# Kernel optimization log

Measured on AMD Instinct MI355X. Metric: run time of the kernel, lower is better.

Reference implementation:

```python
import jax, jax.numpy as jnp
import numpy as np

WIN = 9  # window_size (isotropic, module default)
EPS = 1e-5


def _box_sum3d(x, win):
    """Sum over a win^3 box, same-size output ('same' padding). x: [B,1,D,H,W].
    The ones kernel is separable, so apply three 1D convolutions."""
    pad = win // 2
    for ax in range(3):  # spatial axes D,H,W
        kshape = [1, 1, 1, 1, 1]
        kshape[2 + ax] = win
        k = jnp.ones(kshape, x.dtype)
        padding = [(0, 0)] * 3
        padding[ax] = (pad, pad)
        x = jax.lax.conv_general_dilated(x, k, window_strides=(1, 1, 1), padding=padding)
    return x


def setup_inputs() -> dict:
    key = jax.random.key(0)
    k1, k2 = jax.random.split(key)
    shape = (2, 1, 160, 192, 160)
    y_pred = jax.random.normal(k1, shape, dtype=jnp.float32)
    y_true = jax.random.normal(k2, shape, dtype=jnp.float32)
    return {"y_pred": y_pred, "y_true": y_true}


def reference(y_pred, y_true):
    I, J = y_true, y_pred
    win_size = jnp.asarray(WIN ** 3, I.dtype)  # 729

    I_sum = _box_sum3d(I, WIN)
    J_sum = _box_sum3d(J, WIN)
    I2_sum = _box_sum3d(I * I, WIN)
    J2_sum = _box_sum3d(J * J, WIN)
    IJ_sum = _box_sum3d(I * J, WIN)

    I_mean = I_sum / win_size
    J_mean = J_sum / win_size

    cross = IJ_sum - J_mean * I_sum - I_mean * J_sum + I_mean * J_mean * win_size
    I_var = I2_sum - 2 * I_mean * I_sum + I_mean * I_mean * win_size
    J_var = J2_sum - 2 * J_mean * J_sum + J_mean * J_mean * win_size

    cc = cross * cross / (I_var * J_var + EPS)
    return -jnp.mean(cc)
```

## Files before the change

### kernel.cpp

```cpp
#include <hip/hip_runtime.h>
#include <hip/hip_fp16.h>


#define B_    2
#define D_    160
#define H_    192
#define W_    160
#define HW_   (H_*W_)

#define RS    12
#define SLS   (24*RS)
#define FS    (2*SLS)
#define RAWSZ (5*FS)
#define ZROW  (2*RAWSZ)
#define ZEND  (ZROW + 16)
#define HSUM0 ZEND
#define HCS   160
#define HRS   10
#define HSZ   (10*HCS)
#define REDU  (HSUM0 + 2*HSZ)
#define SMEM  (REDU + 8)
#define DC    80
#define ZCH   (D_/DC)
#define NMAC  ((DC+8)/2)
#define W3I   (1.0f/729.0f)
#define NTOT  9830400.0f

#if __has_builtin(__builtin_amdgcn_rcpf)
#define RCP(x) __builtin_amdgcn_rcpf(x)
#else
#define RCP(x) (1.0f/(x))
#endif

typedef _Float16 half8 __attribute__((ext_vector_type(8)));
typedef float    f32x4 __attribute__((ext_vector_type(4)));
typedef unsigned u32x2 __attribute__((ext_vector_type(2)));
#define MFMA16(a,b,c) __builtin_amdgcn_mfma_f32_16x16x32_f16((a),(b),(c),0,0,0)

#if __has_builtin(__builtin_amdgcn_permlane32_swap)
#define PL32(a,b) do { u32x2 _s = __builtin_amdgcn_permlane32_swap((a),(b),false,false); \
                       (a)=_s[0]; (b)=_s[1]; } while(0)
#else
#define PL32(a,b) asm volatile("s_nop 1\nv_permlane32_swap_b32 %0, %1" : "+v"(a), "+v"(b))
#endif
#if __has_builtin(__builtin_amdgcn_permlane16_swap)
#define PL16(a,b) do { u32x2 _s = __builtin_amdgcn_permlane16_swap((a),(b),false,false); \
                       (a)=_s[0]; (b)=_s[1]; } while(0)
#else
#define PL16(a,b) asm volatile("s_nop 1\nv_permlane16_swap_b32 %0, %1" : "+v"(a), "+v"(b))
#endif

struct __align__(8) HP { __half2 a, b; };

__global__ __launch_bounds__(256, 4) void ncc_fused(const float* __restrict__ gI,
                                                    const float* __restrict__ gJ,
                                                    float* __restrict__ out)
{
  __shared__ __align__(16) float sm[SMEM];
  const int tid  = threadIdx.x;
  const int lane = tid & 63;
  const int Q    = tid >> 6;
  const int n15  = lane & 15;
  const int q4   = lane >> 4;
  const int w0   = blockIdx.x * 16;
  const int h0   = blockIdx.y * 16;
  const int bz   = blockIdx.z;
  const int bb   = bz / ZCH;
  const int d_lo = (bz % ZCH) * DC;

  for (int i = tid; i < ZEND; i += 256) sm[i] = 0.f;

  half8 SEL;
  #pragma unroll
  for (int j = 0; j < 8; ++j) {
    const int k = 8*q4 + j;
    SEL[j] = (k >= n15 && k <= n15 + 8) ? (_Float16)1 : (_Float16)0;
  }

  bool val0 = false, val1 = false;
  int  lo0 = 0, lo1 = 0, sc0 = 0, sc1 = 0;
  const float *pi0 = gI, *pj0 = gJ, *pi1 = gI, *pj1 = gJ;
  {
    auto prep = [&](int t, bool& val, int& lo, int& sc,
                    const float*& pi, const float*& pj) {
      if (t >= 288) { val = false; return; }
      sc = t / 144;
      const int u = t - sc*144;
      const int r = u / 6, c = u - r*6;
      const int gh = h0 - 4 + r, gw = w0 - 4 + 4*c;
      val = ((unsigned)gh < (unsigned)H_) && (gw >= 0) && (gw + 3 < W_);
      lo  = sc*SLS + r*RS + 2*c;
      const long off = ((long)(bb*D_ + (d_lo - 4 + sc))*H_ + gh)*(long)W_ + gw;
      pi = gI + off; pj = gJ + off;
    };
    prep(tid, val0, lo0, sc0, pi0, pj0);
    prep((tid >= 224) ? tid + 32 : 512, val1, lo1, sc1, pi1, pj1);
  }

  int rb_[3], hb_[3];
  #pragma unroll
  for (int i = 0; i < 3; ++i) {
    int c = Q + 4*i; if (c > 9) c = 9;
    rb_[i] = (c % 5)*FS + (c / 5)*SLS;
    hb_[i] = HSUM0 + c*HCS;
  }
  const int a1r = n15*RS + 4*q4;
  const int a2r = (n15 < 8) ? ((16 + n15)*RS + 4*q4) : -1;
  const int zr  = ZROW + 4*q4;

  const int rh = tid >> 4, rw = tid & 15;
  const int rbase = HSUM0 + rw*HRS + (rh >> 1);
  const int rsh   = (rh & 1) * 16;

  float ring[5][9], S[5];
  #pragma unroll
  for (int f = 0; f < 5; ++f) {
    S[f] = 0.f;
    #pragma unroll
    for (int k = 0; k < 9; ++k) ring[f][k] = 0.f;
  }
  float acc = 0.f;

  float4 f0i = {0,0,0,0}, f0j = {0,0,0,0}, f1i = {0,0,0,0}, f1j = {0,0,0,0};
  auto fetch = [&](int sbase) {
    if (val0 && (unsigned)(sbase + sc0) < (unsigned)D_) {
      f0i = *(const float4*)pi0; f0j = *(const float4*)pj0;
    } else { f0i = make_float4(0,0,0,0); f0j = make_float4(0,0,0,0); }
    pi0 += 2*HW_; pj0 += 2*HW_;
    if (val1 && (unsigned)(sbase + sc1) < (unsigned)D_) {
      f1i = *(const float4*)pi1; f1j = *(const float4*)pj1;
    } else { f1i = make_float4(0,0,0,0); f1j = make_float4(0,0,0,0); }
    pi1 += 2*HW_; pj1 += 2*HW_;
  };

  auto stage_one = [&](int lo, float4 fi, float4 fj) {
    const __half2 i01 = __floats2half2_rn(fi.x, fi.y);
    const __half2 i23 = __floats2half2_rn(fi.z, fi.w);
    const __half2 j01 = __floats2half2_rn(fj.x, fj.y);
    const __half2 j23 = __floats2half2_rn(fj.z, fj.w);
    HP hI; hI.a = i01; hI.b = i23;
    HP hJ; hJ.a = j01; hJ.b = j23;
    HP h2; h2.a = __hmul2(i01, i01); h2.b = __hmul2(i23, i23);
    HP h3; h3.a = __hmul2(j01, j01); h3.b = __hmul2(j23, j23);
    HP h4; h4.a = __hmul2(i01, j01); h4.b = __hmul2(i23, j23);
    *(HP*)&sm[lo]        = hI;
    *(HP*)&sm[lo +   FS] = hJ;
    *(HP*)&sm[lo + 2*FS] = h2;
    *(HP*)&sm[lo + 3*FS] = h3;
    *(HP*)&sm[lo + 4*FS] = h4;
  };
  auto stage_write = [&](int buf) {
    const int b = buf * RAWSZ;
    if (val0) stage_one(b + lo0, f0i, f0j);
    if (val1) stage_one(b + lo1, f1i, f1j);
  };

  auto chain = [&](int rb, int hb) {
    const half8 A1 = *(const half8*)&sm[rb + a1r];
    const half8 A2 = (a2r >= 0) ? *(const half8*)&sm[rb + a2r]
                                : *(const half8*)&sm[zr];
    const f32x4 z = {0.f, 0.f, 0.f, 0.f};
    const f32x4 d1 = MFMA16(A1, SEL, z);
    const f32x4 d2 = MFMA16(A2, SEL, z);
    unsigned t0 = __builtin_bit_cast(unsigned, __floats2half2_rn(d1[0], d1[1]));
    unsigned t1 = __builtin_bit_cast(unsigned, __floats2half2_rn(d1[2], d1[3]));
    unsigned u0 = __builtin_bit_cast(unsigned, __floats2half2_rn(d2[0], d2[1]));
    unsigned u1 = __builtin_bit_cast(unsigned, __floats2half2_rn(d2[2], d2[3]));
    PL32(t0, u0);
    PL32(t1, u1);
    PL16(t0, u0);
    PL16(t1, u1);
    union { unsigned u[4]; half8 h; } Bv;
    Bv.u[0] = t0; Bv.u[1] = t1; Bv.u[2] = u0; Bv.u[3] = u1;
    const f32x4 dh = MFMA16(SEL, Bv.h, z);
    HP ph; ph.a = __floats2half2_rn(dh[0], dh[1]); ph.b = __floats2half2_rn(dh[2], dh[3]);
    *(HP*)&sm[hb + n15*HRS + 2*q4] = ph;
  };

  auto h2ext = [&](int addr) -> float {
    const unsigned u = *(const unsigned*)&sm[addr];
    return __half2float(__ushort_as_half((unsigned short)(u >> rsh)));
  };
  auto ring_cc = [&](int m, int hB) {
    float nA[5], nB[5];
    #pragma unroll
    for (int f = 0; f < 5; ++f) {
      nA[f] = h2ext(rbase + hB + f*HCS);
      nB[f] = h2ext(rbase + hB + (5 + f)*HCS);
    }
    float SA[5], SB[5];
    #pragma unroll
    for (int f = 0; f < 5; ++f) {
      SA[f] = S[f]  + nA[f] - ring[f][8];
      SB[f] = SA[f] + nB[f] - ring[f][7];
      S[f]  = SB[f];
      #pragma unroll
      for (int k = 8; k >= 2; --k) ring[f][k] = ring[f][k-2];
      ring[f][1] = nA[f]; ring[f][0] = nB[f];
    }
    if (m >= 4) {
      {
        const float cr = SA[4] - SA[0]*SA[1]*W3I;
        const float vi = SA[2] - SA[0]*SA[0]*W3I;
        const float vj = SA[3] - SA[1]*SA[1]*W3I;
        acc += cr*cr * RCP(vi*vj + 1e-5f);
      }
      {
        const float cr = SB[4] - SB[0]*SB[1]*W3I;
        const float vi = SB[2] - SB[0]*SB[0]*W3I;
        const float vj = SB[3] - SB[1]*SB[1]*W3I;
        acc += cr*cr * RCP(vi*vj + 1e-5f);
      }
    }
  };

  fetch(d_lo - 4);
  __syncthreads();
  stage_write(0);
  fetch(d_lo - 2);
  __syncthreads();

  for (int m = 0; m < NMAC; ++m) {
    const int rB = (m & 1) * RAWSZ;
    const int hB = (m & 1) * HSZ;
    if (m + 1 < NMAC) { stage_write((m + 1) & 1); fetch(d_lo + 2*m); }
    chain(rB + rb_[0], hB + hb_[0]);
    chain(rB + rb_[1], hB + hb_[1]);
    if (Q < 2) chain(rB + rb_[2], hB + hb_[2]);
    __syncthreads();
    ring_cc(m, hB);
  }

  float v = acc;
  #pragma unroll
  for (int off = 32; off > 0; off >>= 1)
    v += __shfl_down(v, off, 64);
  if (lane == 0) sm[REDU + Q] = v;
  __syncthreads();
  if (tid == 0) {
    const float t = sm[REDU] + sm[REDU+1] + sm[REDU+2] + sm[REDU+3];
    atomicAdd(out, -t / NTOT);
  }
}

extern "C" void kernel_launch(void* const* d_in, const int* in_sizes, int n_in,
                              void* d_out, int out_size, void* d_ws, size_t ws_size,
                              hipStream_t stream) {
  const float* J = (const float*)d_in[0];
  const float* I = (const float*)d_in[1];
  float* outp = (float*)d_out;
  hipMemsetAsync(d_out, 0, sizeof(float), stream);
  dim3 grid(W_/16, H_/16, B_*ZCH);
  ncc_fused<<<grid, dim3(256), 0, stream>>>(I, J, outp);
}
```

Baseline: 140.4 us.

## Software-pipeline ring accumulation one step behind MFMA chains to drop a barrier

Restructures the main depth loop so each iteration runs the MFMA box-sum chains for step m while loading and accumulating the previous step's H/W sums from LDS, then stages the next raw slab. The ring-sum and NCC evaluation now lag by one iteration, with a peeled prologue and epilogue, so only one barrier per iteration separates producers from consumers. The aim is to overlap LDS reads and scalar ring work with MFMA latency and to remove the serialisation after the barrier. The cost is more live registers and reliance on the double-buffered hsum region staying valid across the barrier.

```diff
diff --git a/kernel.cpp b/kernel.cpp
--- a/kernel.cpp
+++ b/kernel.cpp
@@ -177,16 +177,19 @@
     *(HP*)&sm[hb + n15*HRS + 2*q4] = ph;
   };
 
-  auto h2ext = [&](int addr) -> float {
-    const unsigned u = *(const unsigned*)&sm[addr];
-    return __half2float(__ushort_as_half((unsigned short)(u >> rsh)));
-  };
-  auto ring_cc = [&](int m, int hB) {
+  auto ring_load = [&](int hB, unsigned* ra, unsigned* rb2) {
+    #pragma unroll
+    for (int f = 0; f < 5; ++f) {
+      ra[f]  = *(const unsigned*)&sm[rbase + hB + f*HCS];
+      rb2[f] = *(const unsigned*)&sm[rbase + hB + (5 + f)*HCS];
+    }
+  };
+  auto ring_fin = [&](int mm, const unsigned* ra, const unsigned* rb2) {
     float nA[5], nB[5];
     #pragma unroll
     for (int f = 0; f < 5; ++f) {
-      nA[f] = h2ext(rbase + hB + f*HCS);
-      nB[f] = h2ext(rbase + hB + (5 + f)*HCS);
+      nA[f] = __half2float(__ushort_as_half((unsigned short)(ra[f]  >> rsh)));
+      nB[f] = __half2float(__ushort_as_half((unsigned short)(rb2[f] >> rsh)));
     }
     float SA[5], SB[5];
     #pragma unroll
@@ -198,7 +201,7 @@
       for (int k = 8; k >= 2; --k) ring[f][k] = ring[f][k-2];
       ring[f][1] = nA[f]; ring[f][0] = nB[f];
     }
-    if (m >= 4) {
+    if (mm >= 4) {
       {
         const float cr = SA[4] - SA[0]*SA[1]*W3I;
         const float vi = SA[2] - SA[0]*SA[0]*W3I;
@@ -220,15 +223,30 @@
   fetch(d_lo - 2);
   __syncthreads();
 
-  for (int m = 0; m < NMAC; ++m) {
+  chain(rb_[0], hb_[0]);
+  chain(rb_[1], hb_[1]);
+  if (Q < 2) chain(rb_[2], hb_[2]);
+  stage_write(1);
+  fetch(d_lo + 0);
+  __syncthreads();
+
+  for (int m = 1; m < NMAC; ++m) {
     const int rB = (m & 1) * RAWSZ;
     const int hB = (m & 1) * HSZ;
-    if (m + 1 < NMAC) { stage_write((m + 1) & 1); fetch(d_lo + 2*m); }
+    const int hP = ((m - 1) & 1) * HSZ;
+    unsigned rgA[5], rgB[5];
     chain(rB + rb_[0], hB + hb_[0]);
+    ring_load(hP, rgA, rgB);
     chain(rB + rb_[1], hB + hb_[1]);
     if (Q < 2) chain(rB + rb_[2], hB + hb_[2]);
+    ring_fin(m - 1, rgA, rgB);
+    if (m + 1 < NMAC) { stage_write((m + 1) & 1); fetch(d_lo + 2*m); }
     __syncthreads();
-    ring_cc(m, hB);
+  }
+  {
+    unsigned rgA[5], rgB[5];
+    ring_load(((NMAC - 1) & 1) * HSZ, rgA, rgB);
+    ring_fin(NMAC - 1, rgA, rgB);
   }
 
   float v = acc;
```

Measured after the change: 139.9 us. About the same (-0.3%).
